# Kernel tuning notes

Hardware: AMD Instinct MI355X
Metric: run time of the kernel (lower is better)

## Reference

```python
import jax, jax.numpy as jnp
import numpy as np

NEG_INF = -1e9  # additive mask value for masked softmax


def setup_inputs() -> dict:
    key = jax.random.key(0)
    k1, k2, k3, k4, k5 = jax.random.split(key, 5)
    bz, rv_num, rv_len, in_feat, out_feat = 32, 10, 128, 300, 128
    seq_a = jax.random.normal(k1, (bz, rv_num, rv_len, in_feat), dtype=jnp.float32)
    seq_b = jax.random.normal(k2, (bz, rv_num, rv_len, in_feat), dtype=jnp.float32)
    mask_a = jax.random.randint(k3, (bz, rv_num, rv_len), 0, 2, dtype=jnp.int32)
    mask_b = jax.random.randint(k4, (bz, rv_num, rv_len), 0, 2, dtype=jnp.int32)
    # guarantee at least one valid position per review (avoid fully-masked rows)
    mask_a = mask_a.at[:, :, 0].set(1)
    mask_b = mask_b.at[:, :, 0].set(1)
    # FC transform params (xavier-normal-ish weight, zero bias)
    W = jax.random.normal(k5, (in_feat, out_feat), dtype=jnp.float32) * (2.0 / np.sqrt(in_feat + out_feat))
    b = jnp.zeros((out_feat,), dtype=jnp.float32)
    return {"seq_a": seq_a, "seq_b": seq_b, "mask_a": mask_a, "mask_b": mask_b, "W": W, "b": b}


def _masked_softmax(scores, mask):
    # scores: [N, L], mask: [N, L] in {0,1}
    logits = jnp.where(mask > 0, scores, NEG_INF)
    return jax.nn.softmax(logits, axis=-1)


def reference(seq_a, seq_b, mask_a, mask_b, W, b):
    bz, rv_num, rv_len, _ = seq_a.shape
    hdim = W.shape[1]
    N = bz * rv_num          # flattened batch of reviews
    M = rv_num * rv_len      # all tokens on the other side

    # FC + ReLU feature transform
    ta = jax.nn.relu(jnp.einsum('bnld,dh->bnlh', seq_a, W) + b)
    tb = jax.nn.relu(jnp.einsum('bnld,dh->bnlh', seq_b, W) + b)

    sa = ta.reshape(N, rv_len, hdim)
    sb = tb.reshape(N, rv_len, hdim)
    # expand: each review attends over ALL tokens of the other sequence in its sample
    ea = jnp.broadcast_to(ta.reshape(bz, 1, M, hdim), (bz, rv_num, M, hdim)).reshape(N, M, hdim)
    eb = jnp.broadcast_to(tb.reshape(bz, 1, M, hdim), (bz, rv_num, M, hdim)).reshape(N, M, hdim)

    # DOT interaction (no scale): affinity [N, rv_len, M]
    atob_aff = jnp.einsum('nld,nmd->nlm', sa, eb)
    btoa_aff = jnp.einsum('nld,nmd->nlm', sb, ea)

    # MEAN pooling over the other-sequence axis
    atob_scores = atob_aff.mean(axis=-1)  # [N, rv_len]
    btoa_scores = btoa_aff.mean(axis=-1)

    ma = mask_a.reshape(N, rv_len)
    mb = mask_b.reshape(N, rv_len)
    atob_w = _masked_softmax(atob_scores, ma)
    btoa_w = _masked_softmax(btoa_scores, mb)

    a_out = jnp.einsum('nl,nld->nd', atob_w, sa)
    b_out = jnp.einsum('nl,nld->nd', btoa_w, sb)
    return (a_out, b_out, atob_w, btoa_w)
```

## Files before the change

### kernel.cpp

```cpp
#include <hip/hip_runtime.h>
#include <hip/hip_bf16.h>


#define K_FEAT 300
#define H 128
#define NTOK 40960
#define NREV 320
#define TOK_PER_SAMPLE 1280
#define TM 128
#define BLKS_PER_SAMPLE 10
#define LDA 40
#define NCHUNK 10
#define WFRAG_ELEMS (NCHUNK * 4 * 4 * 64 * 8)

typedef __attribute__((ext_vector_type(8))) short bf16x8;
typedef __attribute__((ext_vector_type(4))) float f32x4;
typedef unsigned short u16;
typedef unsigned int u32;

static __device__ __forceinline__ u16 f2bf(float x) {
    u32 u = __float_as_uint(x);
    return (u16)((u + 0x7fffu + ((u >> 16) & 1u)) >> 16);
}
static __device__ __forceinline__ float bf2f(u16 s) {
    return __uint_as_float(((u32)s) << 16);
}

__global__ void wsplit_kernel(const float* __restrict__ W, u16* __restrict__ Wfrag)
{
    int i = blockIdx.x * 256 + threadIdx.x;
    if (i >= WFRAG_ELEMS) return;
    int j    = i & 7;
    int lane = (i >> 3) & 63;
    int frag = (i >> 9) & 3;
    int wave = (i >> 11) & 3;
    int c    = i >> 13;
    int nn = lane & 15, quad = lane >> 4;
    int t2 = frag >> 1, part = frag & 1;
    int h = (2 * wave + t2) * 16 + nn;
    int k = c * 32 + quad * 8 + j;
    float w = (k < K_FEAT) ? W[(size_t)k * H + h] : 0.f;
    u16 hi = f2bf(w);
    Wfrag[i] = part ? f2bf(w - bf2f(hi)) : hi;
}

__global__ __launch_bounds__(256, 3) void fc_mfma_kernel(
    const float* __restrict__ seq_a, const float* __restrict__ seq_b,
    const u16* __restrict__ Wfrag, const float* __restrict__ bias,
    u16* __restrict__ ta, u16* __restrict__ tb,
    float* __restrict__ psum_a, float* __restrict__ psum_b)
{
    __shared__ u16 Ah_s[TM * LDA];
    __shared__ u16 Al_s[TM * LDA];
    __shared__ float bias_s[H];

    int blk = blockIdx.x;
    const float* seq; u16* outp; float* psum;
    if (blk < 320) { seq = seq_a; outp = ta; psum = psum_a; }
    else           { seq = seq_b; outp = tb; psum = psum_b; blk -= 320; }

    const int tid = threadIdx.x;
    const int tok0 = blk * TM;
    const int wave = tid >> 6;
    const int lane = tid & 63;
    const int nn = lane & 15;
    const int quad = lane >> 4;

    if (tid < H) bias_s[tid] = bias[tid];

    const int st_t = tid >> 3;
    const int st_j = tid & 7;

    f32x4 acc[8][2];
#pragma unroll
    for (int m = 0; m < 8; ++m) {
        acc[m][0] = (f32x4){0.f, 0.f, 0.f, 0.f};
        acc[m][1] = (f32x4){0.f, 0.f, 0.f, 0.f};
    }

    float4 pf[4];
#pragma unroll
    for (int it = 0; it < 4; ++it) {
        int t = st_t + it * 32;
        int kk = 4 * st_j;
        pf[it] = make_float4(0.f, 0.f, 0.f, 0.f);
        if (kk + 4 <= K_FEAT)
            pf[it] = *(const float4*)&seq[(size_t)(tok0 + t) * K_FEAT + kk];
    }
#pragma unroll
    for (int it = 0; it < 4; ++it) {
        int t = st_t + it * 32;
        float4 v = pf[it];
        u16 h0 = f2bf(v.x), h1 = f2bf(v.y), h2 = f2bf(v.z), h3 = f2bf(v.w);
        uint2 hp, lp;
        hp.x = (u32)h0 | ((u32)h1 << 16);
        hp.y = (u32)h2 | ((u32)h3 << 16);
        lp.x = (u32)f2bf(v.x - bf2f(h0)) | ((u32)f2bf(v.y - bf2f(h1)) << 16);
        lp.y = (u32)f2bf(v.z - bf2f(h2)) | ((u32)f2bf(v.w - bf2f(h3)) << 16);
        *(uint2*)&Ah_s[t * LDA + 4 * st_j] = hp;
        *(uint2*)&Al_s[t * LDA + 4 * st_j] = lp;
    }
    __syncthreads();

    for (int c = 0; c < NCHUNK; ++c) {
        if (c < NCHUNK - 1) {
#pragma unroll
            for (int it = 0; it < 4; ++it) {
                int t = st_t + it * 32;
                int kk = (c + 1) * 32 + 4 * st_j;
                pf[it] = make_float4(0.f, 0.f, 0.f, 0.f);
                if (kk + 4 <= K_FEAT)
                    pf[it] = *(const float4*)&seq[(size_t)(tok0 + t) * K_FEAT + kk];
            }
        }
        const u16* wf = Wfrag + (size_t)(c * 4 + wave) * 2048;
        bf16x8 bh0 = *(const bf16x8*)&wf[0 * 512 + lane * 8];
        bf16x8 bl0 = *(const bf16x8*)&wf[1 * 512 + lane * 8];
        bf16x8 bh1 = *(const bf16x8*)&wf[2 * 512 + lane * 8];
        bf16x8 bl1 = *(const bf16x8*)&wf[3 * 512 + lane * 8];
#pragma unroll
        for (int m = 0; m < 8; ++m) {
            bf16x8 a_hi = *(const bf16x8*)&Ah_s[(m * 16 + nn) * LDA + quad * 8];
            bf16x8 a_lo = *(const bf16x8*)&Al_s[(m * 16 + nn) * LDA + quad * 8];
            acc[m][0] = __builtin_amdgcn_mfma_f32_16x16x32_bf16(bh0, a_hi, acc[m][0], 0, 0, 0);
            acc[m][0] = __builtin_amdgcn_mfma_f32_16x16x32_bf16(bl0, a_hi, acc[m][0], 0, 0, 0);
            acc[m][0] = __builtin_amdgcn_mfma_f32_16x16x32_bf16(bh0, a_lo, acc[m][0], 0, 0, 0);
            acc[m][1] = __builtin_amdgcn_mfma_f32_16x16x32_bf16(bh1, a_hi, acc[m][1], 0, 0, 0);
            acc[m][1] = __builtin_amdgcn_mfma_f32_16x16x32_bf16(bl1, a_hi, acc[m][1], 0, 0, 0);
            acc[m][1] = __builtin_amdgcn_mfma_f32_16x16x32_bf16(bh1, a_lo, acc[m][1], 0, 0, 0);
        }
        __syncthreads();
        if (c < NCHUNK - 1) {
#pragma unroll
            for (int it = 0; it < 4; ++it) {
                int t = st_t + it * 32;
                float4 v = pf[it];
                u16 h0 = f2bf(v.x), h1 = f2bf(v.y), h2 = f2bf(v.z), h3 = f2bf(v.w);
                uint2 hp, lp;
                hp.x = (u32)h0 | ((u32)h1 << 16);
                hp.y = (u32)h2 | ((u32)h3 << 16);
                lp.x = (u32)f2bf(v.x - bf2f(h0)) | ((u32)f2bf(v.y - bf2f(h1)) << 16);
                lp.y = (u32)f2bf(v.z - bf2f(h2)) | ((u32)f2bf(v.w - bf2f(h3)) << 16);
                *(uint2*)&Ah_s[t * LDA + 4 * st_j] = hp;
                *(uint2*)&Al_s[t * LDA + 4 * st_j] = lp;
            }
            __syncthreads();
        }
    }

#pragma unroll
    for (int ht = 0; ht < 2; ++ht) {
        int h0 = (2 * wave + ht) * 16 + quad * 4;
        float4 bb = *(const float4*)&bias_s[h0];
        float fs[4] = {0.f, 0.f, 0.f, 0.f};
#pragma unroll
        for (int tt = 0; tt < 8; ++tt) {
            int tok = tok0 + tt * 16 + nn;
            float v0 = fmaxf(acc[tt][ht][0] + bb.x, 0.f);
            float v1 = fmaxf(acc[tt][ht][1] + bb.y, 0.f);
            float v2 = fmaxf(acc[tt][ht][2] + bb.z, 0.f);
            float v3 = fmaxf(acc[tt][ht][3] + bb.w, 0.f);
            fs[0] += v0; fs[1] += v1; fs[2] += v2; fs[3] += v3;
            uint2 p;
            p.x = (u32)f2bf(v0) | ((u32)f2bf(v1) << 16);
            p.y = (u32)f2bf(v2) | ((u32)f2bf(v3) << 16);
            *(uint2*)&outp[(size_t)tok * H + h0] = p;
        }
#pragma unroll
        for (int r = 0; r < 4; ++r) {
            fs[r] += __shfl_xor(fs[r], 1);
            fs[r] += __shfl_xor(fs[r], 2);
            fs[r] += __shfl_xor(fs[r], 4);
            fs[r] += __shfl_xor(fs[r], 8);
        }
        if (nn == 0) {
#pragma unroll
            for (int r = 0; r < 4; ++r)
                psum[(size_t)blk * H + h0 + r] = fs[r];
        }
    }
}

__global__ __launch_bounds__(256) void attn_kernel(
    const u16* __restrict__ ta, const u16* __restrict__ tb,
    const int* __restrict__ mask_a, const int* __restrict__ mask_b,
    const float* __restrict__ psum_a, const float* __restrict__ psum_b,
    float* __restrict__ out)
{
    int n = blockIdx.x;
    int side = 0;
    if (n >= NREV) { side = 1; n -= NREV; }

    const u16* t = side ? tb : ta;
    const int* mask = side ? mask_b : mask_a;
    const float* psum_o = side ? psum_a : psum_b;
    float* out_vec = out + (side ? NREV * H : 0);
    float* out_w = out + 2 * NREV * H + (side ? NREV * H : 0);

    int sample = n / 10;
    int tid = threadIdx.x;

    __shared__ float score_part[128 * 17];
    __shared__ float mean_s[128];
    __shared__ float w_s[128];
    __shared__ float red[4];
    __shared__ float part_out[16 * 128];

    if (tid < 128) {
        float s = 0.f;
        const float* pb = psum_o + (size_t)sample * BLKS_PER_SAMPLE * H + tid;
#pragma unroll
        for (int i = 0; i < BLKS_PER_SAMPLE; ++i) s += pb[(size_t)i * H];
        mean_s[tid] = s * (1.0f / (float)TOK_PER_SAMPLE);
    }
    __syncthreads();

    const u16* rowbase = t + (size_t)n * 128 * H;

#pragma unroll
    for (int i = 0; i < 8; ++i) {
        int q = tid + 256 * i;
        int r = q >> 4;
        int c8 = q & 15;
        uint4 v = *(const uint4*)&rowbase[r * H + c8 * 8];
        const float* m = &mean_s[c8 * 8];
        float p = 0.f;
        p += bf2f((u16)(v.x & 0xffff)) * m[0];
        p += bf2f((u16)(v.x >> 16)) * m[1];
        p += bf2f((u16)(v.y & 0xffff)) * m[2];
        p += bf2f((u16)(v.y >> 16)) * m[3];
        p += bf2f((u16)(v.z & 0xffff)) * m[4];
        p += bf2f((u16)(v.z >> 16)) * m[5];
        p += bf2f((u16)(v.w & 0xffff)) * m[6];
        p += bf2f((u16)(v.w >> 16)) * m[7];
        score_part[r * 17 + c8] = p;
    }
    __syncthreads();

    float logit = -1e9f;
    if (tid < 128) {
        float s = 0.f;
#pragma unroll
        for (int j = 0; j < 16; ++j) s += score_part[tid * 17 + j];
        int mv = mask[n * 128 + tid];
        logit = (mv > 0) ? s : -1e9f;
    }

    float mx = logit;
    for (int off = 32; off > 0; off >>= 1) mx = fmaxf(mx, __shfl_xor(mx, off));
    if ((tid & 63) == 0) red[tid >> 6] = mx;
    __syncthreads();
    mx = fmaxf(fmaxf(red[0], red[1]), fmaxf(red[2], red[3]));
    __syncthreads();

    float e = __expf(logit - mx);
    float ssum = e;
    for (int off = 32; off > 0; off >>= 1) ssum += __shfl_xor(ssum, off);
    if ((tid & 63) == 0) red[tid >> 6] = ssum;
    __syncthreads();
    ssum = red[0] + red[1] + red[2] + red[3];

    float w = e / ssum;
    if (tid < 128) {
        w_s[tid] = w;
        out_w[n * 128 + tid] = w;
    }
    __syncthreads();

    int c8 = tid & 15;
    int lp = tid >> 4;
    float o[8] = {0.f, 0.f, 0.f, 0.f, 0.f, 0.f, 0.f, 0.f};
#pragma unroll
    for (int k = 0; k < 8; ++k) {
        int l = k * 16 + lp;
        float wl = w_s[l];
        uint4 v = *(const uint4*)&rowbase[l * H + c8 * 8];
        o[0] = fmaf(wl, bf2f((u16)(v.x & 0xffff)), o[0]);
        o[1] = fmaf(wl, bf2f((u16)(v.x >> 16)), o[1]);
        o[2] = fmaf(wl, bf2f((u16)(v.y & 0xffff)), o[2]);
        o[3] = fmaf(wl, bf2f((u16)(v.y >> 16)), o[3]);
        o[4] = fmaf(wl, bf2f((u16)(v.z & 0xffff)), o[4]);
        o[5] = fmaf(wl, bf2f((u16)(v.z >> 16)), o[5]);
        o[6] = fmaf(wl, bf2f((u16)(v.w & 0xffff)), o[6]);
        o[7] = fmaf(wl, bf2f((u16)(v.w >> 16)), o[7]);
    }
    *(float4*)&part_out[lp * 128 + c8 * 8] = make_float4(o[0], o[1], o[2], o[3]);
    *(float4*)&part_out[lp * 128 + c8 * 8 + 4] = make_float4(o[4], o[5], o[6], o[7]);
    __syncthreads();
    if (tid < 128) {
        float s = 0.f;
#pragma unroll
        for (int p = 0; p < 16; ++p) s += part_out[p * 128 + tid];
        out_vec[n * 128 + tid] = s;
    }
}

extern "C" void kernel_launch(void* const* d_in, const int* in_sizes, int n_in,
                              void* d_out, int out_size, void* d_ws, size_t ws_size,
                              hipStream_t stream)
{
    const float* seq_a = (const float*)d_in[0];
    const float* seq_b = (const float*)d_in[1];
    const int* mask_a = (const int*)d_in[2];
    const int* mask_b = (const int*)d_in[3];
    const float* W = (const float*)d_in[4];
    const float* bias = (const float*)d_in[5];
    float* out = (float*)d_out;

    u16* ta = (u16*)d_ws;
    u16* tb = ta + (size_t)NTOK * H;
    float* psum_a = (float*)(tb + (size_t)NTOK * H);
    float* psum_b = psum_a + NREV * H;
    u16* Wfrag = (u16*)(psum_b + NREV * H);

    wsplit_kernel<<<(WFRAG_ELEMS + 255) / 256, 256, 0, stream>>>(W, Wfrag);
    fc_mfma_kernel<<<640, 256, 0, stream>>>(seq_a, seq_b, Wfrag, bias, ta, tb, psum_a, psum_b);
    attn_kernel<<<640, 256, 0, stream>>>(ta, tb, mask_a, mask_b, psum_a, psum_b, out);
}
```

Baseline: 162.5 us.

## Halve FC tile, double-buffer LDS chunks, and widen attention blocks to 512 threads

```diff
diff --git a/kernel.cpp b/kernel.cpp
--- a/kernel.cpp
+++ b/kernel.cpp
@@ -7,8 +7,9 @@
 #define NTOK 40960
 #define NREV 320
 #define TOK_PER_SAMPLE 1280
-#define TM 128
-#define BLKS_PER_SAMPLE 10
+#define TM 64
+#define FC_BLKS_PER_SIDE 640
+#define FC_BLKS_PER_SAMPLE 20
 #define LDA 40
 #define NCHUNK 10
 #define WFRAG_ELEMS (NCHUNK * 4 * 4 * 64 * 8)
@@ -44,20 +45,20 @@
     Wfrag[i] = part ? f2bf(w - bf2f(hi)) : hi;
 }
 
-__global__ __launch_bounds__(256, 3) void fc_mfma_kernel(
+__global__ __launch_bounds__(256, 5) void fc_mfma_kernel(
     const float* __restrict__ seq_a, const float* __restrict__ seq_b,
     const u16* __restrict__ Wfrag, const float* __restrict__ bias,
     u16* __restrict__ ta, u16* __restrict__ tb,
     float* __restrict__ psum_a, float* __restrict__ psum_b)
 {
-    __shared__ u16 Ah_s[TM * LDA];
-    __shared__ u16 Al_s[TM * LDA];
+    __shared__ u16 Ah_s[2][TM * LDA];
+    __shared__ u16 Al_s[2][TM * LDA];
     __shared__ float bias_s[H];
 
     int blk = blockIdx.x;
     const float* seq; u16* outp; float* psum;
-    if (blk < 320) { seq = seq_a; outp = ta; psum = psum_a; }
-    else           { seq = seq_b; outp = tb; psum = psum_b; blk -= 320; }
+    if (blk < FC_BLKS_PER_SIDE) { seq = seq_a; outp = ta; psum = psum_a; }
+    else { seq = seq_b; outp = tb; psum = psum_b; blk -= FC_BLKS_PER_SIDE; }
 
     const int tid = threadIdx.x;
     const int tok0 = blk * TM;
@@ -71,24 +72,21 @@
     const int st_t = tid >> 3;
     const int st_j = tid & 7;
 
-    f32x4 acc[8][2];
-#pragma unroll
-    for (int m = 0; m < 8; ++m) {
+    f32x4 acc[4][2];
+#pragma unroll
+    for (int m = 0; m < 4; ++m) {
         acc[m][0] = (f32x4){0.f, 0.f, 0.f, 0.f};
         acc[m][1] = (f32x4){0.f, 0.f, 0.f, 0.f};
     }
 
-    float4 pf[4];
-#pragma unroll
-    for (int it = 0; it < 4; ++it) {
+    float4 pf[2];
+#pragma unroll
+    for (int it = 0; it < 2; ++it) {
         int t = st_t + it * 32;
-        int kk = 4 * st_j;
-        pf[it] = make_float4(0.f, 0.f, 0.f, 0.f);
-        if (kk + 4 <= K_FEAT)
-            pf[it] = *(const float4*)&seq[(size_t)(tok0 + t) * K_FEAT + kk];
-    }
-#pragma unroll
-    for (int it = 0; it < 4; ++it) {
+        pf[it] = *(const float4*)&seq[(size_t)(tok0 + t) * K_FEAT + 4 * st_j];
+    }
+#pragma unroll
+    for (int it = 0; it < 2; ++it) {
         int t = st_t + it * 32;
         float4 v = pf[it];
         u16 h0 = f2bf(v.x), h1 = f2bf(v.y), h2 = f2bf(v.z), h3 = f2bf(v.w);
@@ -97,15 +95,17 @@
         hp.y = (u32)h2 | ((u32)h3 << 16);
         lp.x = (u32)f2bf(v.x - bf2f(h0)) | ((u32)f2bf(v.y - bf2f(h1)) << 16);
         lp.y = (u32)f2bf(v.z - bf2f(h2)) | ((u32)f2bf(v.w - bf2f(h3)) << 16);
-        *(uint2*)&Ah_s[t * LDA + 4 * st_j] = hp;
-        *(uint2*)&Al_s[t * LDA + 4 * st_j] = lp;
-    }
-    __syncthreads();
-
+        *(uint2*)&Ah_s[0][t * LDA + 4 * st_j] = hp;
+        *(uint2*)&Al_s[0][t * LDA + 4 * st_j] = lp;
+    }
+    __syncthreads();
+
+#pragma unroll
     for (int c = 0; c < NCHUNK; ++c) {
+        const int cur = c & 1;
         if (c < NCHUNK - 1) {
 #pragma unroll
-            for (int it = 0; it < 4; ++it) {
+            for (int it = 0; it < 2; ++it) {
                 int t = st_t + it * 32;
                 int kk = (c + 1) * 32 + 4 * st_j;
                 pf[it] = make_float4(0.f, 0.f, 0.f, 0.f);
@@ -119,9 +119,9 @@
         bf16x8 bh1 = *(const bf16x8*)&wf[2 * 512 + lane * 8];
         bf16x8 bl1 = *(const bf16x8*)&wf[3 * 512 + lane * 8];
 #pragma unroll
-        for (int m = 0; m < 8; ++m) {
-            bf16x8 a_hi = *(const bf16x8*)&Ah_s[(m * 16 + nn) * LDA + quad * 8];
-            bf16x8 a_lo = *(const bf16x8*)&Al_s[(m * 16 + nn) * LDA + quad * 8];
+        for (int m = 0; m < 4; ++m) {
+            bf16x8 a_hi = *(const bf16x8*)&Ah_s[cur][(m * 16 + nn) * LDA + quad * 8];
+            bf16x8 a_lo = *(const bf16x8*)&Al_s[cur][(m * 16 + nn) * LDA + quad * 8];
             acc[m][0] = __builtin_amdgcn_mfma_f32_16x16x32_bf16(bh0, a_hi, acc[m][0], 0, 0, 0);
             acc[m][0] = __builtin_amdgcn_mfma_f32_16x16x32_bf16(bl0, a_hi, acc[m][0], 0, 0, 0);
             acc[m][0] = __builtin_amdgcn_mfma_f32_16x16x32_bf16(bh0, a_lo, acc[m][0], 0, 0, 0);
@@ -129,10 +129,9 @@
             acc[m][1] = __builtin_amdgcn_mfma_f32_16x16x32_bf16(bl1, a_hi, acc[m][1], 0, 0, 0);
             acc[m][1] = __builtin_amdgcn_mfma_f32_16x16x32_bf16(bh1, a_lo, acc[m][1], 0, 0, 0);
         }
-        __syncthreads();
         if (c < NCHUNK - 1) {
 #pragma unroll
-            for (int it = 0; it < 4; ++it) {
+            for (int it = 0; it < 2; ++it) {
                 int t = st_t + it * 32;
                 float4 v = pf[it];
                 u16 h0 = f2bf(v.x), h1 = f2bf(v.y), h2 = f2bf(v.z), h3 = f2bf(v.w);
@@ -141,8 +140,8 @@
                 hp.y = (u32)h2 | ((u32)h3 << 16);
                 lp.x = (u32)f2bf(v.x - bf2f(h0)) | ((u32)f2bf(v.y - bf2f(h1)) << 16);
                 lp.y = (u32)f2bf(v.z - bf2f(h2)) | ((u32)f2bf(v.w - bf2f(h3)) << 16);
-                *(uint2*)&Ah_s[t * LDA + 4 * st_j] = hp;
-                *(uint2*)&Al_s[t * LDA + 4 * st_j] = lp;
+                *(uint2*)&Ah_s[cur ^ 1][t * LDA + 4 * st_j] = hp;
+                *(uint2*)&Al_s[cur ^ 1][t * LDA + 4 * st_j] = lp;
             }
             __syncthreads();
         }
@@ -154,7 +153,7 @@
         float4 bb = *(const float4*)&bias_s[h0];
         float fs[4] = {0.f, 0.f, 0.f, 0.f};
 #pragma unroll
-        for (int tt = 0; tt < 8; ++tt) {
+        for (int tt = 0; tt < 4; ++tt) {
             int tok = tok0 + tt * 16 + nn;
             float v0 = fmaxf(acc[tt][ht][0] + bb.x, 0.f);
             float v1 = fmaxf(acc[tt][ht][1] + bb.y, 0.f);
@@ -181,7 +180,7 @@
     }
 }
 
-__global__ __launch_bounds__(256) void attn_kernel(
+__global__ __launch_bounds__(512) void attn_kernel(
     const u16* __restrict__ ta, const u16* __restrict__ tb,
     const int* __restrict__ mask_a, const int* __restrict__ mask_b,
     const float* __restrict__ psum_a, const float* __restrict__ psum_b,
@@ -203,14 +202,14 @@
     __shared__ float score_part[128 * 17];
     __shared__ float mean_s[128];
     __shared__ float w_s[128];
-    __shared__ float red[4];
-    __shared__ float part_out[16 * 128];
+    __shared__ float red[8];
+    __shared__ float part_out[32 * 128];
 
     if (tid < 128) {
         float s = 0.f;
-        const float* pb = psum_o + (size_t)sample * BLKS_PER_SAMPLE * H + tid;
-#pragma unroll
-        for (int i = 0; i < BLKS_PER_SAMPLE; ++i) s += pb[(size_t)i * H];
+        const float* pb = psum_o + (size_t)sample * FC_BLKS_PER_SAMPLE * H + tid;
+#pragma unroll
+        for (int i = 0; i < FC_BLKS_PER_SAMPLE; ++i) s += pb[(size_t)i * H];
         mean_s[tid] = s * (1.0f / (float)TOK_PER_SAMPLE);
     }
     __syncthreads();
@@ -218,8 +217,8 @@
     const u16* rowbase = t + (size_t)n * 128 * H;
 
 #pragma unroll
-    for (int i = 0; i < 8; ++i) {
-        int q = tid + 256 * i;
+    for (int i = 0; i < 4; ++i) {
+        int q = tid + 512 * i;
         int r = q >> 4;
         int c8 = q & 15;
         uint4 v = *(const uint4*)&rowbase[r * H + c8 * 8];
@@ -250,7 +249,9 @@
     for (int off = 32; off > 0; off >>= 1) mx = fmaxf(mx, __shfl_xor(mx, off));
     if ((tid & 63) == 0) red[tid >> 6] = mx;
     __syncthreads();
-    mx = fmaxf(fmaxf(red[0], red[1]), fmaxf(red[2], red[3]));
+    mx = red[0];
+#pragma unroll
+    for (int rr = 1; rr < 8; ++rr) mx = fmaxf(mx, red[rr]);
     __syncthreads();
 
     float e = __expf(logit - mx);
@@ -258,7 +259,9 @@
     for (int off = 32; off > 0; off >>= 1) ssum += __shfl_xor(ssum, off);
     if ((tid & 63) == 0) red[tid >> 6] = ssum;
     __syncthreads();
-    ssum = red[0] + red[1] + red[2] + red[3];
+    ssum = 0.f;
+#pragma unroll
+    for (int rr = 0; rr < 8; ++rr) ssum += red[rr];
 
     float w = e / ssum;
     if (tid < 128) {
@@ -271,8 +274,8 @@
     int lp = tid >> 4;
     float o[8] = {0.f, 0.f, 0.f, 0.f, 0.f, 0.f, 0.f, 0.f};
 #pragma unroll
-    for (int k = 0; k < 8; ++k) {
-        int l = k * 16 + lp;
+    for (int k = 0; k < 4; ++k) {
+        int l = k * 32 + lp;
         float wl = w_s[l];
         uint4 v = *(const uint4*)&rowbase[l * H + c8 * 8];
         o[0] = fmaf(wl, bf2f((u16)(v.x & 0xffff)), o[0]);
@@ -290,7 +293,7 @@
     if (tid < 128) {
         float s = 0.f;
 #pragma unroll
-        for (int p = 0; p < 16; ++p) s += part_out[p * 128 + tid];
+        for (int p = 0; p < 32; ++p) s += part_out[p * 128 + tid];
         out_vec[n * 128 + tid] = s;
     }
 }
@@ -310,10 +313,10 @@
     u16* ta = (u16*)d_ws;
     u16* tb = ta + (size_t)NTOK * H;
     float* psum_a = (float*)(tb + (size_t)NTOK * H);
-    float* psum_b = psum_a + NREV * H;
-    u16* Wfrag = (u16*)(psum_b + NREV * H);
+    float* psum_b = psum_a + FC_BLKS_PER_SIDE * H;
+    u16* Wfrag = (u16*)(psum_b + FC_BLKS_PER_SIDE * H);
 
     wsplit_kernel<<<(WFRAG_ELEMS + 255) / 256, 256, 0, stream>>>(W, Wfrag);
-    fc_mfma_kernel<<<640, 256, 0, stream>>>(seq_a, seq_b, Wfrag, bias, ta, tb, psum_a, psum_b);
-    attn_kernel<<<640, 256, 0, stream>>>(ta, tb, mask_a, mask_b, psum_a, psum_b, out);
-}
+    fc_mfma_kernel<<<2 * FC_BLKS_PER_SIDE, 256, 0, stream>>>(seq_a, seq_b, Wfrag, bias, ta, tb, psum_a, psum_b);
+    attn_kernel<<<640, 512, 0, stream>>>(ta, tb, mask_a, mask_b, psum_a, psum_b, out);
+}
```

Result: faster. 150.6 us (-7.3%).
